# Kernel tuning notes

Measured on AMD Instinct MI355X. Metric: run time of the kernel, lower is better.

The kernel has to match this reference:

```python
import jax, jax.numpy as jnp
import numpy as np

B, T, IN, OUT, H, N, M = 16, 1024, 64, 64, 512, 128, 40
EPS = 1e-8


def setup_inputs() -> dict:
    key = jax.random.key(0)
    ks = jax.random.split(key, 16)
    s = 0.02  # xavier-ish init scale for weights
    inp = {
        "x": jax.random.normal(ks[0], (B, T, IN), jnp.float32),
        "h0": jnp.zeros((B, H), jnp.float32),
        "c0": jnp.zeros((B, H), jnp.float32),
        "memory0": jax.random.normal(ks[1], (B, N, M), jnp.float32) * 0.01,
        "read0": jnp.zeros((B, M), jnp.float32),
        # LSTMCell params (torch gate order: i, f, g, o)
        "W_ih": jax.random.normal(ks[2], (4 * H, IN + M), jnp.float32) * s,
        "b_ih": jnp.zeros((4 * H,), jnp.float32),
        "W_hh": jax.random.normal(ks[3], (4 * H, H), jnp.float32) * s,
        "b_hh": jnp.zeros((4 * H,), jnp.float32),
        "W_fc": jax.random.normal(ks[4], (OUT, H), jnp.float32) * s,
        "b_fc": jnp.zeros((OUT,), jnp.float32),
        "W_e": jax.random.normal(ks[5], (M, H), jnp.float32) * s,
        "b_e": jnp.zeros((M,), jnp.float32),
        "W_a": jax.random.normal(ks[6], (M, H), jnp.float32) * s,
        "b_a": jnp.zeros((M,), jnp.float32),
        "W_k": jax.random.normal(ks[7], (M, H), jnp.float32) * s,
        "b_k": jnp.zeros((M,), jnp.float32),
        "W_b": jax.random.normal(ks[8], (1, H), jnp.float32) * s,
        "b_b": jnp.zeros((1,), jnp.float32),
    }
    return inp


def _ntm_scan(x, h0, c0, memory0, read0, W_ih, b_ih, W_hh, b_hh,
              W_fc, b_fc, W_e, b_e, W_a, b_a, W_k, b_k, W_b, b_b):
    def step(carry, x_t):
        h, c, mem, r = carry
        # controller LSTM cell on [x_t, read_vector]
        inp = jnp.concatenate([x_t, r], axis=-1)            # [B, IN+M]
        gates = inp @ W_ih.T + b_ih + h @ W_hh.T + b_hh      # [B, 4H]
        i, f, g, o = jnp.split(gates, 4, axis=-1)
        i = jax.nn.sigmoid(i); f = jax.nn.sigmoid(f)
        g = jnp.tanh(g);       o = jax.nn.sigmoid(o)
        c = f * c + i * g
        h = o * jnp.tanh(c)
        out = jnp.tanh(h @ W_fc.T + b_fc)                    # [B, OUT]
        # content addressing
        key = jnp.tanh(h @ W_k.T + b_k)                      # [B, M]
        beta = jax.nn.softplus(h @ W_b.T + b_b) + EPS        # [B, 1]
        kn = key / (jnp.linalg.norm(key, axis=-1, keepdims=True) + EPS)
        mn = mem / (jnp.linalg.norm(mem, axis=-1, keepdims=True) + EPS)
        sim = jnp.einsum('bnm,bm->bn', mn, kn)               # [B, N]
        w = jax.nn.softmax(beta * sim, axis=-1)              # [B, N]
        # erase/add write, then read from updated memory
        e = jax.nn.sigmoid(h @ W_e.T + b_e)                  # [B, M]
        a = jnp.tanh(h @ W_a.T + b_a)                        # [B, M]
        mem = mem * (1.0 - w[:, :, None] * e[:, None, :]) + w[:, :, None] * a[:, None, :]
        r = jnp.einsum('bn,bnm->bm', w, mem)                 # [B, M]
        return (h, c, mem, r), out

    xs = jnp.swapaxes(x, 0, 1)                               # [T, B, IN]
    (h, c, mem, r), outs = jax.lax.scan(step, (h0, c0, memory0, read0), xs)
    return jnp.swapaxes(outs, 0, 1), h, c                    # [B, T, OUT]


def reference(x, h0, c0, memory0, read0, W_ih, b_ih, W_hh, b_hh,
              W_fc, b_fc, W_e, b_e, W_a, b_a, W_k, b_k, W_b, b_b):
    return _ntm_scan(x, h0, c0, memory0, read0, W_ih, b_ih, W_hh, b_hh,
                     W_fc, b_fc, W_e, b_e, W_a, b_a, W_k, b_k, W_b, b_b)
```

## Files before the change

### kernel.cpp

```cpp
#include <hip/hip_runtime.h>
#include <math.h>

#define Bq   16
#define Tq   1024
#define INq  64
#define OUTq 64
#define Hq   512
#define Nq   128
#define Mq   40
#define SP   580
#define NWGATE 128
#define NWMEM  16
#define NWG    144
#define NT     512
#define EPSq 1e-8f

typedef unsigned long long ull;

__device__ __forceinline__ float sigmf(float x){ return 1.f/(1.f + expf(-x)); }
__device__ __forceinline__ float softplusf(float x){ return (x > 20.f) ? x : log1pf(expf(x)); }

__device__ __forceinline__ ull icld64(const ull* p){
  return __hip_atomic_load(p, __ATOMIC_RELAXED, __HIP_MEMORY_SCOPE_AGENT);
}
__device__ __forceinline__ void icst64(ull* p, ull v){
  __hip_atomic_store(p, v, __ATOMIC_RELAXED, __HIP_MEMORY_SCOPE_AGENT);
}
__device__ __forceinline__ ull packtv(unsigned tag, float v){
  return ((ull)tag << 32) | (ull)__float_as_uint(v);
}
__device__ __forceinline__ float lowf(ull v){ return __uint_as_float((unsigned)v); }

extern "C" __global__ void __launch_bounds__(NT, 1)
ntm_kernel(const float* __restrict__ xg,  const float* __restrict__ h0g,
           const float* __restrict__ c0g, const float* __restrict__ mem0g,
           const float* __restrict__ read0g,
           const float* __restrict__ Wih, const float* __restrict__ bih,
           const float* __restrict__ Whh, const float* __restrict__ bhh,
           const float* __restrict__ Wfc, const float* __restrict__ bfc,
           const float* __restrict__ We,  const float* __restrict__ be,
           const float* __restrict__ Wa,  const float* __restrict__ ba,
           const float* __restrict__ Wk,  const float* __restrict__ bk,
           const float* __restrict__ Wb,  const float* __restrict__ bbeta,
           float* __restrict__ yout, ull* __restrict__ h_tag,
           ull* __restrict__ r_rep, ull* __restrict__ h_okr)
{
  const int wg  = blockIdx.x;
  const int tid = threadIdx.x;
  __shared__ __align__(16) char smem[60992];

  if (wg < NWGATE){
    float* inp_s  = (float*)smem;
    float* red_s  = (float*)(smem + 37120);
    float* r_s    = (float*)(smem + 54528);
    float* gate_s = (float*)(smem + 57344);
    float* c_s    = (float*)(smem + 58368);
    float* bias_s = (float*)(smem + 58624);
    float* ored_s = (float*)(smem + 58688);

    const int kseg = tid & 15;
    const int rg   = (tid >> 4) & 3;
    const int bg   = tid >> 6;
    const int rep  = wg & 7;

    float4 w4[36];
    #pragma unroll
    for (int g = 0; g < 4; ++g){
      const int row = g*Hq + wg*4 + rg;
      #pragma unroll
      for (int kk = 0; kk < 9; ++kk){
        float v[4];
        #pragma unroll
        for (int c4 = 0; c4 < 4; ++c4){
          const int k = kseg*36 + kk*4 + c4;
          v[c4] = (k < 64) ? Wih[row*104 + k] : Whh[row*512 + (k - 64)];
        }
        w4[g*9 + kk] = make_float4(v[0], v[1], v[2], v[3]);
      }
    }
    float4 wr[10];
    if (tid < 256){
      const int l = tid & 15;
      const int row = (l >> 2)*Hq + wg*4 + (l & 3);
      const float* wir = Wih + row*104 + 64;
      #pragma unroll
      for (int q = 0; q < 10; ++q) wr[q] = *(const float4*)&wir[q*4];
    }
    float4 wf[4]; float bfcv = 0.f;
    if (wg < 64){
      const int ks = tid & 31;
      #pragma unroll
      for (int q = 0; q < 4; ++q)
        wf[q] = *(const float4*)&Wfc[wg*Hq + ks*16 + q*4];
      bfcv = bfc[wg];
    }
    if (tid < 16){
      const int row = (tid >> 2)*Hq + wg*4 + (tid & 3);
      bias_s[tid] = bih[row] + bhh[row];
    }
    if (tid < 64){ const int hh = tid & 3, b = tid >> 2;
      c_s[hh*16 + b] = c0g[b*Hq + wg*4 + hh]; }
    {
      const float4* x4 = (const float4*)xg;
      if (tid < 256){ const int b = tid >> 4, q = tid & 15;
        *(float4*)&inp_s[b*SP + q*4] = x4[(b*Tq + 0)*16 + q]; }
      const float4* h4 = (const float4*)h0g;
      #pragma unroll
      for (int j = 0; j < 4; ++j){ const int i4 = tid + 512*j;
        const int b = i4 >> 7, q = i4 & 127;
        *(float4*)&inp_s[b*SP + 64 + q*4] = h4[b*128 + q]; }
    }
    __syncthreads();

    for (int t = 0; t < Tq; ++t){
      {
        float acc[4][2] = {};
        const float* base = inp_s + kseg*36;
        #pragma unroll
        for (int bl = 0; bl < 2; ++bl){
          const float* bp = base + (2*bg + bl)*SP;
          #pragma unroll
          for (int kk = 0; kk < 9; ++kk){
            const float4 f = *(const float4*)&bp[kk*4];
            #pragma unroll
            for (int g = 0; g < 4; ++g){
              acc[g][bl] += w4[g*9+kk].x*f.x + w4[g*9+kk].y*f.y
                          + w4[g*9+kk].z*f.z + w4[g*9+kk].w*f.w;
            }
          }
        }
        #pragma unroll
        for (int bl = 0; bl < 2; ++bl)
          #pragma unroll
          for (int g = 0; g < 4; ++g)
            red_s[((2*bg + bl)*16 + g*4 + rg)*17 + kseg] = acc[g][bl];
      }
      __syncthreads();
      float part = 0.f;
      if (tid < 256){
        part = bias_s[tid & 15];
        const float* rp = &red_s[tid*17];
        #pragma unroll
        for (int j = 0; j < 16; ++j) part += rp[j];
      }
      if (t == 0){
        if (tid < 320){ const int b = tid/20, mp = tid - b*20;
          *(float2*)&r_s[b*44 + mp*2] = *(const float2*)&read0g[b*40 + mp*2]; }
      } else if (tid < 320){
        const unsigned want = (unsigned)t;
        const ull* rt = r_rep + (ull)(rep*2 + ((t-1)&1))*640;
        ull v1 = icld64(&rt[tid]);
        ull v2 = icld64(&rt[tid + 320]);
        while (((unsigned)(v1 >> 32) != want) | ((unsigned)(v2 >> 32) != want)){
          __builtin_amdgcn_s_sleep(2);
          v1 = icld64(&rt[tid]);
          v2 = icld64(&rt[tid + 320]);
        }
        { const int b = tid/40, m = tid - b*40;       r_s[b*44 + m] = lowf(v1); }
        { const int w = tid + 320, b = w/40, m = w - b*40; r_s[b*44 + m] = lowf(v2); }
      }
      __syncthreads();
      if (tid < 256){
        const int fb = tid >> 4;
        float s = part;
        #pragma unroll
        for (int q = 0; q < 10; ++q){
          const float4 rv = *(const float4*)&r_s[fb*44 + q*4];
          s += wr[q].x*rv.x + wr[q].y*rv.y + wr[q].z*rv.z + wr[q].w*rv.w;
        }
        gate_s[fb*16 + (tid & 15)] = s;
      }
      __syncthreads();
      if (tid < 64){
        const int hh = tid & 3, b = tid >> 2;
        const float gi = gate_s[b*16 + hh];
        const float gf = gate_s[b*16 + 4 + hh];
        const float gc = gate_s[b*16 + 8 + hh];
        const float go = gate_s[b*16 + 12 + hh];
        const float iv = sigmf(gi), fv = sigmf(gf), gv = tanhf(gc), ov = sigmf(go);
        const float cn = fv*c_s[hh*16 + b] + iv*gv;
        const float hn = ov*tanhf(cn);
        c_s[hh*16 + b] = cn;
        icst64(&h_tag[((ull)((t&1)*16 + b))*512 + wg*4 + hh],
               packtv((unsigned)(t+1), hn));
        if (t == Tq - 1){
          yout[Bq*Tq*OUTq + b*Hq + wg*4 + hh] = hn;
          yout[Bq*Tq*OUTq + Bq*Hq + b*Hq + wg*4 + hh] = cn;
        }
      }
      if (wg < 64 && t > 0){
        const int ob = tid >> 5, ks = tid & 31;
        float p = 0.f;
        const float* hp = &inp_s[ob*SP + 64 + ks*16];
        #pragma unroll
        for (int q = 0; q < 4; ++q){
          const float4 f = *(const float4*)&hp[q*4];
          p += wf[q].x*f.x + wf[q].y*f.y + wf[q].z*f.z + wf[q].w*f.w;
        }
        ored_s[ob*36 + ks] = p;
      }
      {
        const unsigned want = (unsigned)(t+1);
        if (tid < 16){
          const ull* fp = &h_okr[(ull)(rep*2 + (t&1))*16 + tid];
          while ((unsigned)(icld64(fp) >> 32) != want)
            __builtin_amdgcn_s_sleep(2);
        }
        __syncthreads();
        const ull* ht = h_tag + (ull)(t&1)*8192;
        ull v[16];
        #pragma unroll
        for (int j = 0; j < 16; ++j) v[j] = icld64(&ht[tid + 512*j]);
        if (wg < 64 && t > 0 && tid < 16){
          const float* op = &ored_s[tid*36];
          float s = bfcv;
          #pragma unroll
          for (int j = 0; j < 32; ++j) s += op[j];
          yout[(tid*Tq + (t-1))*OUTq + wg] = tanhf(s);
        }
        #pragma unroll
        for (int j = 0; j < 16; ++j)
          inp_s[j*SP + 64 + tid] = lowf(v[j]);
      }
      if (t + 1 < Tq && tid < 256){
        const float4* x4 = (const float4*)xg;
        const int b = tid >> 4, q = tid & 15;
        *(float4*)&inp_s[b*SP + q*4] = x4[(b*Tq + (t + 1))*16 + q];
      }
      __syncthreads();
    }
    if (wg < 64){
      const int ob = tid >> 5, ks = tid & 31;
      float p = 0.f;
      const float* hp = &inp_s[ob*SP + 64 + ks*16];
      #pragma unroll
      for (int q = 0; q < 4; ++q){
        const float4 f = *(const float4*)&hp[q*4];
        p += wf[q].x*f.x + wf[q].y*f.y + wf[q].z*f.z + wf[q].w*f.w;
      }
      ored_s[ob*36 + ks] = p;
      __syncthreads();
      if (tid < 16){
        const float* op = &ored_s[tid*36];
        float s = bfcv;
        #pragma unroll
        for (int j = 0; j < 32; ++j) s += op[j];
        yout[(tid*Tq + (Tq-1))*OUTq + wg] = tanhf(s);
      }
    }
  }
  else {
    const int bat = wg - NWGATE;
    float* mem_s  = (float*)smem;
    float* h_s    = (float*)(smem + 22528);
    float* hred_s = (float*)(smem + 24576);
    float* key_s  = (float*)(smem + 26624);
    float* e_s    = (float*)(smem + 26784);
    float* a_s    = (float*)(smem + 26944);
    float* w_s    = (float*)(smem + 27104);
    float* rred_s = (float*)(smem + 27616);

    #pragma unroll
    for (int j = 0; j < 10; ++j){
      const int e = j*512 + tid;
      const int n = e / 40, m = e - n*40;
      mem_s[n*44 + m] = mem0g[bat*(Nq*Mq) + e];
    }
    const int o  = tid & 127;
    const int kc = tid >> 7;
    const float* wrow = (o < 40) ? (Wk + o*Hq)
                      : (o < 80) ? (We + (o-40)*Hq)
                      : (o < 120) ? (Wa + (o-80)*Hq)
                      : (o == 120) ? Wb : nullptr;
    float4 wv2[32];
    if (wrow){
      #pragma unroll
      for (int kk = 0; kk < 32; ++kk)
        wv2[kk] = *(const float4*)&wrow[kc*128 + kk*4];
    } else {
      #pragma unroll
      for (int kk = 0; kk < 32; ++kk) wv2[kk] = make_float4(0.f,0.f,0.f,0.f);
    }
    float hb0 = 0.f, hb1 = 0.f;
    if (tid < 64){
      const int o0 = tid, o1 = tid + 64;
      hb0 = (o0 < 40) ? bk[o0] : be[o0-40];
      hb1 = (o1 < 80) ? be[o1-40] : (o1 < 120) ? ba[o1-80]
          : (o1 == 120) ? bbeta[0] : 0.f;
    }
    __syncthreads();

    for (int t = 0; t < Tq; ++t){
      const int p = t & 1;
      const unsigned want = (unsigned)(t+1);
      {
        const ull* ht = h_tag + ((ull)(p*16 + bat))*512;
        ull v;
        do { v = icld64(&ht[tid]); } while ((unsigned)(v >> 32) != want);
        h_s[tid] = lowf(v);
      }
      __syncthreads();
      if (tid < 8)
        icst64(&h_okr[(ull)(tid*2 + p)*16 + bat], packtv(want, 0.f));
      {
        float a0 = 0.f;
        const float* hp = h_s + kc*128;
        #pragma unroll
        for (int kk = 0; kk < 32; ++kk){
          const float4 f = *(const float4*)&hp[kk*4];
          a0 += wv2[kk].x*f.x + wv2[kk].y*f.y + wv2[kk].z*f.z + wv2[kk].w*f.w;
        }
        hred_s[o*4 + kc] = a0;
      }
      __syncthreads();
      if (tid < 64){
        const int l = tid;
        const float4 p0 = *(const float4*)&hred_s[l*4];
        const float4 p1 = *(const float4*)&hred_s[(l+64)*4];
        float s0 = hb0 + p0.x + p0.y + p0.z + p0.w;
        float s1 = hb1 + p1.x + p1.y + p1.z + p1.w;
        float kv = 0.f;
        if (l < 40){ kv = tanhf(s0); key_s[l] = kv; }
        else        { e_s[l-40] = sigmf(s0); }
        if (l < 16)      e_s[l+24]  = sigmf(s1);
        else if (l < 56) a_s[l-16]  = tanhf(s1);
        float bval = softplusf(s1) + EPSq;
        const float bet = __shfl(bval, 56);
        float ss = kv*kv;
        #pragma unroll
        for (int off = 32; off; off >>= 1) ss += __shfl_xor(ss, off);
        const float rinv = 1.f/(sqrtf(ss) + EPSq);
        float sc[2];
        #pragma unroll
        for (int half = 0; half < 2; ++half){
          const int n = l + 64*half;
          float qq = 0.f, dd = 0.f;
          const float* mrow = &mem_s[n*44];
          #pragma unroll
          for (int q = 0; q < 10; ++q){
            const float4 mv = *(const float4*)&mrow[q*4];
            const float4 kvv = *(const float4*)&key_s[q*4];
            qq += mv.x*mv.x + mv.y*mv.y + mv.z*mv.z + mv.w*mv.w;
            dd += mv.x*kvv.x + mv.y*kvv.y + mv.z*kvv.z + mv.w*kvv.w;
          }
          sc[half] = bet * dd * rinv / (sqrtf(qq) + EPSq);
        }
        float mx = fmaxf(sc[0], sc[1]);
        #pragma unroll
        for (int off = 32; off; off >>= 1) mx = fmaxf(mx, __shfl_xor(mx, off));
        const float e0 = expf(sc[0] - mx), e1 = expf(sc[1] - mx);
        float sm = e0 + e1;
        #pragma unroll
        for (int off = 32; off; off >>= 1) sm += __shfl_xor(sm, off);
        const float inv = 1.f/sm;
        w_s[l] = e0*inv; w_s[l+64] = e1*inv;
      }
      __syncthreads();
      if (tid < 320){
        const int m = tid % 40, ng = tid / 40;
        const float ev = e_s[m], av = a_s[m];
        float part = 0.f;
        #pragma unroll
        for (int j = 0; j < 16; ++j){
          const int n = ng*16 + j, idx = n*44 + m;
          const float mv = mem_s[idx];
          const float wn = w_s[n];
          const float nv = fmaf(wn, fmaf(-ev, mv, av), mv);
          mem_s[idx] = nv;
          part = fmaf(wn, nv, part);
        }
        rred_s[m*9 + ng] = part;
      }
      __syncthreads();
      if (tid < 40){
        float r = 0.f;
        #pragma unroll
        for (int j = 0; j < 8; ++j) r += rred_s[tid*9 + j];
        const ull pv = packtv(want, r);
        #pragma unroll
        for (int rp2 = 0; rp2 < 8; ++rp2)
          icst64(&r_rep[(ull)(rp2*2 + p)*640 + bat*40 + tid], pv);
      }
    }
  }
}

extern "C" void kernel_launch(void* const* d_in, const int* in_sizes, int n_in,
                              void* d_out, int out_size, void* d_ws, size_t ws_size,
                              hipStream_t stream){
  const float* xg    = (const float*)d_in[0];
  const float* h0g   = (const float*)d_in[1];
  const float* c0g   = (const float*)d_in[2];
  const float* mem0g = (const float*)d_in[3];
  const float* read0g= (const float*)d_in[4];
  const float* Wih   = (const float*)d_in[5];
  const float* bih   = (const float*)d_in[6];
  const float* Whh   = (const float*)d_in[7];
  const float* bhh   = (const float*)d_in[8];
  const float* Wfc   = (const float*)d_in[9];
  const float* bfc   = (const float*)d_in[10];
  const float* We    = (const float*)d_in[11];
  const float* be    = (const float*)d_in[12];
  const float* Wa    = (const float*)d_in[13];
  const float* ba    = (const float*)d_in[14];
  const float* Wk    = (const float*)d_in[15];
  const float* bk    = (const float*)d_in[16];
  const float* Wb    = (const float*)d_in[17];
  const float* bbeta = (const float*)d_in[18];

  float* yout  = (float*)d_out;
  ull*   h_tag = (ull*)d_ws;
  ull*   r_rep = (ull*)((char*)d_ws + 131072);
  ull*   h_okr = (ull*)((char*)d_ws + 212992);

  hipMemsetAsync(d_ws, 0, 215040, stream);
  hipLaunchKernelGGL(ntm_kernel, dim3(NWG), dim3(NT), 0, stream,
                     xg, h0g, c0g, mem0g, read0g, Wih, bih, Whh, bhh,
                     Wfc, bfc, We, be, Wa, ba, Wk, bk, Wb, bbeta,
                     yout, h_tag, r_rep, h_okr);
}
```

Measured before the change: 7.000 ms.

## Partition persistent NTM kernel into per-batch islands with local L2 flag exchange

```diff
diff --git a/kernel.cpp b/kernel.cpp
--- a/kernel.cpp
+++ b/kernel.cpp
@@ -3,16 +3,15 @@
 
 #define Bq   16
 #define Tq   1024
-#define INq  64
 #define OUTq 64
 #define Hq   512
 #define Nq   128
 #define Mq   40
-#define SP   580
-#define NWGATE 128
-#define NWMEM  16
-#define NWG    144
-#define NT     512
+#define NT   512
+#define NISL 16
+#define GWG  13
+#define IWG  14
+#define NWG  224
 #define EPSq 1e-8f
 
 typedef unsigned long long ull;
@@ -26,10 +25,34 @@
 __device__ __forceinline__ void icst64(ull* p, ull v){
   __hip_atomic_store(p, v, __ATOMIC_RELAXED, __HIP_MEMORY_SCOPE_AGENT);
 }
+__device__ __forceinline__ ull l2ld64(const ull* p){
+  ull v;
+  asm volatile("global_load_dwordx2 %0, %1, off sc0\n\ts_waitcnt vmcnt(0)"
+               : "=v"(v) : "v"(p) : "memory");
+  return v;
+}
 __device__ __forceinline__ ull packtv(unsigned tag, float v){
   return ((ull)tag << 32) | (ull)__float_as_uint(v);
 }
 __device__ __forceinline__ float lowf(ull v){ return __uint_as_float((unsigned)v); }
+
+__device__ __forceinline__ void publish(ull* loc, ull* sh, ull v){
+  *loc = v;
+  icst64(sh, v);
+}
+__device__ __forceinline__ float waitword(const ull* loc, const ull* sh, unsigned want){
+  #pragma unroll 1
+  for (int i = 0; i < 12; ++i){
+    const ull v = l2ld64(loc);
+    if ((unsigned)(v >> 32) == want) return lowf(v);
+    __builtin_amdgcn_s_sleep(1);
+  }
+  for (;;){
+    const ull v = icld64(sh);
+    if ((unsigned)(v >> 32) == want) return lowf(v);
+    __builtin_amdgcn_s_sleep(2);
+  }
+}
 
 extern "C" __global__ void __launch_bounds__(NT, 1)
 ntm_kernel(const float* __restrict__ xg,  const float* __restrict__ h0g,
@@ -42,215 +65,139 @@
            const float* __restrict__ Wa,  const float* __restrict__ ba,
            const float* __restrict__ Wk,  const float* __restrict__ bk,
            const float* __restrict__ Wb,  const float* __restrict__ bbeta,
-           float* __restrict__ yout, ull* __restrict__ h_tag,
-           ull* __restrict__ r_rep, ull* __restrict__ h_okr)
+           float* __restrict__ yout, ull* __restrict__ rdy,
+           ull* __restrict__ h_loc, ull* __restrict__ h_sh,
+           ull* __restrict__ r_loc, ull* __restrict__ r_sh)
 {
-  const int wg  = blockIdx.x;
+  const int blk = blockIdx.x;
   const int tid = threadIdx.x;
-  __shared__ __align__(16) char smem[60992];
-
-  if (wg < NWGATE){
+  const int x   = blk & 7;
+  const int j   = blk >> 3;
+  const int bat = (j < IWG) ? x : (x + 8);
+  const int slot= (j < IWG) ? j : (j - IWG);
+  __shared__ __align__(16) char smem[41344];
+
+  if (slot < GWG){
     float* inp_s  = (float*)smem;
-    float* red_s  = (float*)(smem + 37120);
-    float* r_s    = (float*)(smem + 54528);
-    float* gate_s = (float*)(smem + 57344);
-    float* c_s    = (float*)(smem + 58368);
-    float* bias_s = (float*)(smem + 58624);
-    float* ored_s = (float*)(smem + 58688);
-
-    const int kseg = tid & 15;
-    const int rg   = (tid >> 4) & 3;
-    const int bg   = tid >> 6;
-    const int rep  = wg & 7;
-
-    float4 w4[36];
+    float* red_s  = (float*)(smem + 2560);
+    float* rw_s   = (float*)(smem + 13440);
+    float* r_s    = (float*)(smem + 39680);
+    float* gate_s = (float*)(smem + 39840);
+    float* c_s    = (float*)(smem + 40480);
+    float* bias_s = (float*)(smem + 40640);
+
+    const int kseg  = tid & 15;
+    const int rslot = tid >> 4;
+    const int nd    = (slot < 12) ? 40 : 32;
+    const int d0    = slot * 40;
+    const int rowsR = 4 * nd;
+
+    float4 w4[5][9];
     #pragma unroll
-    for (int g = 0; g < 4; ++g){
-      const int row = g*Hq + wg*4 + rg;
+    for (int rr = 0; rr < 5; ++rr){
+      const int row = rslot*5 + rr;
+      if (row < rowsR){
+        const int gate = row / nd, ld = row - gate*nd;
+        const int grow = gate*Hq + d0 + ld;
+        #pragma unroll
+        for (int kk = 0; kk < 9; ++kk){
+          float v[4];
+          #pragma unroll
+          for (int c4 = 0; c4 < 4; ++c4){
+            const int k = kseg*36 + kk*4 + c4;
+            v[c4] = (k < 64) ? Wih[grow*104 + k] : Whh[grow*512 + (k - 64)];
+          }
+          w4[rr][kk] = make_float4(v[0], v[1], v[2], v[3]);
+        }
+      } else {
+        #pragma unroll
+        for (int kk = 0; kk < 9; ++kk) w4[rr][kk] = make_float4(0.f,0.f,0.f,0.f);
+      }
+    }
+    if (tid < rowsR){
+      const int gate = tid / nd, ld = tid - gate*nd;
+      const int grow = gate*Hq + d0 + ld;
+      bias_s[tid] = bih[grow] + bhh[grow];
+    }
+    for (int i = tid; i < rowsR*40; i += NT){
+      const int row = i / 40, m = i - row*40;
+      const int gate = row / nd, ld = row - gate*nd;
+      const int grow = gate*Hq + d0 + ld;
+      rw_s[row*41 + m] = Wih[grow*104 + 64 + m];
+    }
+    if (tid < nd) c_s[tid] = c0g[bat*Hq + d0 + tid];
+    if (tid < 16)
+      *(float4*)&inp_s[tid*4] = ((const float4*)xg)[(bat*Tq + 0)*16 + tid];
+    if (tid < 128)
+      *(float4*)&inp_s[64 + tid*4] = ((const float4*)h0g)[bat*128 + tid];
+    __syncthreads();
+    if (tid == 0){
+      __hip_atomic_fetch_add(rdy, 1ull, __ATOMIC_RELAXED, __HIP_MEMORY_SCOPE_AGENT);
+      while (icld64(rdy) < (ull)NWG) __builtin_amdgcn_s_sleep(8);
+    }
+    __syncthreads();
+
+    for (int t = 0; t < Tq; ++t){
+      const int p = t & 1, pm = (t - 1) & 1;
+      float acc[5] = {0.f,0.f,0.f,0.f,0.f};
+      {
+        const float* bp = inp_s + kseg*36;
+        #pragma unroll
+        for (int kk = 0; kk < 9; ++kk){
+          const float4 f = *(const float4*)&bp[kk*4];
+          #pragma unroll
+          for (int rr = 0; rr < 5; ++rr)
+            acc[rr] += w4[rr][kk].x*f.x + w4[rr][kk].y*f.y
+                     + w4[rr][kk].z*f.z + w4[rr][kk].w*f.w;
+        }
+      }
       #pragma unroll
-      for (int kk = 0; kk < 9; ++kk){
-        float v[4];
-        #pragma unroll
-        for (int c4 = 0; c4 < 4; ++c4){
-          const int k = kseg*36 + kk*4 + c4;
-          v[c4] = (k < 64) ? Wih[row*104 + k] : Whh[row*512 + (k - 64)];
-        }
-        w4[g*9 + kk] = make_float4(v[0], v[1], v[2], v[3]);
-      }
-    }
-    float4 wr[10];
-    if (tid < 256){
-      const int l = tid & 15;
-      const int row = (l >> 2)*Hq + wg*4 + (l & 3);
-      const float* wir = Wih + row*104 + 64;
-      #pragma unroll
-      for (int q = 0; q < 10; ++q) wr[q] = *(const float4*)&wir[q*4];
-    }
-    float4 wf[4]; float bfcv = 0.f;
-    if (wg < 64){
-      const int ks = tid & 31;
-      #pragma unroll
-      for (int q = 0; q < 4; ++q)
-        wf[q] = *(const float4*)&Wfc[wg*Hq + ks*16 + q*4];
-      bfcv = bfc[wg];
-    }
-    if (tid < 16){
-      const int row = (tid >> 2)*Hq + wg*4 + (tid & 3);
-      bias_s[tid] = bih[row] + bhh[row];
-    }
-    if (tid < 64){ const int hh = tid & 3, b = tid >> 2;
-      c_s[hh*16 + b] = c0g[b*Hq + wg*4 + hh]; }
-    {
-      const float4* x4 = (const float4*)xg;
-      if (tid < 256){ const int b = tid >> 4, q = tid & 15;
-        *(float4*)&inp_s[b*SP + q*4] = x4[(b*Tq + 0)*16 + q]; }
-      const float4* h4 = (const float4*)h0g;
-      #pragma unroll
-      for (int j = 0; j < 4; ++j){ const int i4 = tid + 512*j;
-        const int b = i4 >> 7, q = i4 & 127;
-        *(float4*)&inp_s[b*SP + 64 + q*4] = h4[b*128 + q]; }
-    }
-    __syncthreads();
-
-    for (int t = 0; t < Tq; ++t){
-      {
-        float acc[4][2] = {};
-        const float* base = inp_s + kseg*36;
-        #pragma unroll
-        for (int bl = 0; bl < 2; ++bl){
-          const float* bp = base + (2*bg + bl)*SP;
-          #pragma unroll
-          for (int kk = 0; kk < 9; ++kk){
-            const float4 f = *(const float4*)&bp[kk*4];
-            #pragma unroll
-            for (int g = 0; g < 4; ++g){
-              acc[g][bl] += w4[g*9+kk].x*f.x + w4[g*9+kk].y*f.y
-                          + w4[g*9+kk].z*f.z + w4[g*9+kk].w*f.w;
-            }
-          }
-        }
-        #pragma unroll
-        for (int bl = 0; bl < 2; ++bl)
-          #pragma unroll
-          for (int g = 0; g < 4; ++g)
-            red_s[((2*bg + bl)*16 + g*4 + rg)*17 + kseg] = acc[g][bl];
-      }
-      __syncthreads();
-      float part = 0.f;
-      if (tid < 256){
-        part = bias_s[tid & 15];
+      for (int rr = 0; rr < 5; ++rr)
+        red_s[(rslot*5 + rr)*17 + kseg] = acc[rr];
+      if (t == 0){
+        if (tid < 40) r_s[tid] = read0g[bat*Mq + tid];
+      } else if (tid < 40){
+        const int idx = (pm*NISL + bat)*Mq + tid;
+        r_s[tid] = waitword(&r_loc[idx], &r_sh[idx], (unsigned)t);
+      }
+      __syncthreads();
+      if (tid < rowsR){
+        float s2 = bias_s[tid];
         const float* rp = &red_s[tid*17];
         #pragma unroll
-        for (int j = 0; j < 16; ++j) part += rp[j];
-      }
-      if (t == 0){
-        if (tid < 320){ const int b = tid/20, mp = tid - b*20;
-          *(float2*)&r_s[b*44 + mp*2] = *(const float2*)&read0g[b*40 + mp*2]; }
-      } else if (tid < 320){
-        const unsigned want = (unsigned)t;
-        const ull* rt = r_rep + (ull)(rep*2 + ((t-1)&1))*640;
-        ull v1 = icld64(&rt[tid]);
-        ull v2 = icld64(&rt[tid + 320]);
-        while (((unsigned)(v1 >> 32) != want) | ((unsigned)(v2 >> 32) != want)){
-          __builtin_amdgcn_s_sleep(2);
-          v1 = icld64(&rt[tid]);
-          v2 = icld64(&rt[tid + 320]);
-        }
-        { const int b = tid/40, m = tid - b*40;       r_s[b*44 + m] = lowf(v1); }
-        { const int w = tid + 320, b = w/40, m = w - b*40; r_s[b*44 + m] = lowf(v2); }
-      }
-      __syncthreads();
-      if (tid < 256){
-        const int fb = tid >> 4;
-        float s = part;
-        #pragma unroll
-        for (int q = 0; q < 10; ++q){
-          const float4 rv = *(const float4*)&r_s[fb*44 + q*4];
-          s += wr[q].x*rv.x + wr[q].y*rv.y + wr[q].z*rv.z + wr[q].w*rv.w;
-        }
-        gate_s[fb*16 + (tid & 15)] = s;
-      }
-      __syncthreads();
-      if (tid < 64){
-        const int hh = tid & 3, b = tid >> 2;
-        const float gi = gate_s[b*16 + hh];
-        const float gf = gate_s[b*16 + 4 + hh];
-        const float gc = gate_s[b*16 + 8 + hh];
-        const float go = gate_s[b*16 + 12 + hh];
+        for (int q = 0; q < 16; ++q) s2 += rp[q];
+        const float* rwp = &rw_s[tid*41];
+        #pragma unroll
+        for (int m = 0; m < 40; ++m) s2 += rwp[m]*r_s[m];
+        gate_s[tid] = s2;
+      }
+      __syncthreads();
+      if (tid < nd){
+        const float gi = gate_s[tid];
+        const float gf = gate_s[nd + tid];
+        const float gc = gate_s[2*nd + tid];
+        const float go = gate_s[3*nd + tid];
         const float iv = sigmf(gi), fv = sigmf(gf), gv = tanhf(gc), ov = sigmf(go);
-        const float cn = fv*c_s[hh*16 + b] + iv*gv;
+        const float cn = fv*c_s[tid] + iv*gv;
         const float hn = ov*tanhf(cn);
-        c_s[hh*16 + b] = cn;
-        icst64(&h_tag[((ull)((t&1)*16 + b))*512 + wg*4 + hh],
-               packtv((unsigned)(t+1), hn));
+        c_s[tid] = cn;
+        const int idx = (p*NISL + bat)*Hq + d0 + tid;
+        publish(&h_loc[idx], &h_sh[idx], packtv((unsigned)(t+1), hn));
         if (t == Tq - 1){
-          yout[Bq*Tq*OUTq + b*Hq + wg*4 + hh] = hn;
-          yout[Bq*Tq*OUTq + Bq*Hq + b*Hq + wg*4 + hh] = cn;
-        }
-      }
-      if (wg < 64 && t > 0){
-        const int ob = tid >> 5, ks = tid & 31;
-        float p = 0.f;
-        const float* hp = &inp_s[ob*SP + 64 + ks*16];
-        #pragma unroll
-        for (int q = 0; q < 4; ++q){
-          const float4 f = *(const float4*)&hp[q*4];
-          p += wf[q].x*f.x + wf[q].y*f.y + wf[q].z*f.z + wf[q].w*f.w;
-        }
-        ored_s[ob*36 + ks] = p;
-      }
-      {
-        const unsigned want = (unsigned)(t+1);
-        if (tid < 16){
-          const ull* fp = &h_okr[(ull)(rep*2 + (t&1))*16 + tid];
-          while ((unsigned)(icld64(fp) >> 32) != want)
-            __builtin_amdgcn_s_sleep(2);
-        }
-        __syncthreads();
-        const ull* ht = h_tag + (ull)(t&1)*8192;
-        ull v[16];
-        #pragma unroll
-        for (int j = 0; j < 16; ++j) v[j] = icld64(&ht[tid + 512*j]);
-        if (wg < 64 && t > 0 && tid < 16){
-          const float* op = &ored_s[tid*36];
-          float s = bfcv;
-          #pragma unroll
-          for (int j = 0; j < 32; ++j) s += op[j];
-          yout[(tid*Tq + (t-1))*OUTq + wg] = tanhf(s);
-        }
-        #pragma unroll
-        for (int j = 0; j < 16; ++j)
-          inp_s[j*SP + 64 + tid] = lowf(v[j]);
-      }
-      if (t + 1 < Tq && tid < 256){
-        const float4* x4 = (const float4*)xg;
-        const int b = tid >> 4, q = tid & 15;
-        *(float4*)&inp_s[b*SP + q*4] = x4[(b*Tq + (t + 1))*16 + q];
-      }
-      __syncthreads();
-    }
-    if (wg < 64){
-      const int ob = tid >> 5, ks = tid & 31;
-      float p = 0.f;
-      const float* hp = &inp_s[ob*SP + 64 + ks*16];
-      #pragma unroll
-      for (int q = 0; q < 4; ++q){
-        const float4 f = *(const float4*)&hp[q*4];
-        p += wf[q].x*f.x + wf[q].y*f.y + wf[q].z*f.z + wf[q].w*f.w;
-      }
-      ored_s[ob*36 + ks] = p;
-      __syncthreads();
-      if (tid < 16){
-        const float* op = &ored_s[tid*36];
-        float s = bfcv;
-        #pragma unroll
-        for (int j = 0; j < 32; ++j) s += op[j];
-        yout[(tid*Tq + (Tq-1))*OUTq + wg] = tanhf(s);
-      }
+          yout[Bq*Tq*OUTq + bat*Hq + d0 + tid] = hn;
+          yout[Bq*Tq*OUTq + Bq*Hq + bat*Hq + d0 + tid] = cn;
+        }
+      }
+      {
+        const int idx = (p*NISL + bat)*Hq + tid;
+        inp_s[64 + tid] = waitword(&h_loc[idx], &h_sh[idx], (unsigned)(t+1));
+      }
+      if (t + 1 < Tq && tid < 16)
+        *(float4*)&inp_s[tid*4] = ((const float4*)xg)[(bat*Tq + t + 1)*16 + tid];
+      __syncthreads();
     }
   }
   else {
-    const int bat = wg - NWGATE;
     float* mem_s  = (float*)smem;
     float* h_s    = (float*)(smem + 22528);
     float* hred_s = (float*)(smem + 24576);
@@ -259,10 +206,11 @@
     float* a_s    = (float*)(smem + 26944);
     float* w_s    = (float*)(smem + 27104);
     float* rred_s = (float*)(smem + 27616);
+    float* ored_s = (float*)(smem + 29056);
 
     #pragma unroll
-    for (int j = 0; j < 10; ++j){
-      const int e = j*512 + tid;
+    for (int q = 0; q < 10; ++q){
+      const int e = q*512 + tid;
       const int n = e / 40, m = e - n*40;
       mem_s[n*44 + m] = mem0g[bat*(Nq*Mq) + e];
     }
@@ -281,6 +229,14 @@
       #pragma unroll
       for (int kk = 0; kk < 32; ++kk) wv2[kk] = make_float4(0.f,0.f,0.f,0.f);
     }
+    float4 wfc[16];
+    {
+      const int o2 = tid & 63, kc8 = tid >> 6;
+      #pragma unroll
+      for (int kk = 0; kk < 16; ++kk)
+        wfc[kk] = *(const float4*)&Wfc[o2*Hq + kc8*64 + kk*4];
+    }
+    const float bfcv = bfc[tid & 63];
     float hb0 = 0.f, hb1 = 0.f;
     if (tid < 64){
       const int o0 = tid, o1 = tid + 64;
@@ -289,19 +245,20 @@
           : (o1 == 120) ? bbeta[0] : 0.f;
     }
     __syncthreads();
+    if (tid == 0){
+      __hip_atomic_fetch_add(rdy, 1ull, __ATOMIC_RELAXED, __HIP_MEMORY_SCOPE_AGENT);
+      while (icld64(rdy) < (ull)NWG) __builtin_amdgcn_s_sleep(8);
+    }
+    __syncthreads();
 
     for (int t = 0; t < Tq; ++t){
       const int p = t & 1;
-      const unsigned want = (unsigned)(t+1);
-      {
-        const ull* ht = h_tag + ((ull)(p*16 + bat))*512;
-        ull v;
-        do { v = icld64(&ht[tid]); } while ((unsigned)(v >> 32) != want);
-        h_s[tid] = lowf(v);
-      }
-      __syncthreads();
-      if (tid < 8)
-        icst64(&h_okr[(ull)(tid*2 + p)*16 + bat], packtv(want, 0.f));
+      const unsigned want = (unsigned)(t + 1);
+      {
+        const int idx = (p*NISL + bat)*Hq + tid;
+        h_s[tid] = waitword(&h_loc[idx], &h_sh[idx], want);
+      }
+      __syncthreads();
       {
         float a0 = 0.f;
         const float* hp = h_s + kc*128;
@@ -361,12 +318,12 @@
         const float ev = e_s[m], av = a_s[m];
         float part = 0.f;
         #pragma unroll
-        for (int j = 0; j < 16; ++j){
-          const int n = ng*16 + j, idx = n*44 + m;
-          const float mv = mem_s[idx];
+        for (int q = 0; q < 16; ++q){
+          const int n = ng*16 + q, idx2 = n*44 + m;
+          const float mv = mem_s[idx2];
           const float wn = w_s[n];
           const float nv = fmaf(wn, fmaf(-ev, mv, av), mv);
-          mem_s[idx] = nv;
+          mem_s[idx2] = nv;
           part = fmaf(wn, nv, part);
         }
         rred_s[m*9 + ng] = part;
@@ -375,12 +332,30 @@
       if (tid < 40){
         float r = 0.f;
         #pragma unroll
-        for (int j = 0; j < 8; ++j) r += rred_s[tid*9 + j];
-        const ull pv = packtv(want, r);
-        #pragma unroll
-        for (int rp2 = 0; rp2 < 8; ++rp2)
-          icst64(&r_rep[(ull)(rp2*2 + p)*640 + bat*40 + tid], pv);
-      }
+        for (int q = 0; q < 8; ++q) r += rred_s[tid*9 + q];
+        const int idx = (p*NISL + bat)*Mq + tid;
+        publish(&r_loc[idx], &r_sh[idx], packtv(want, r));
+      }
+      {
+        const int o2 = tid & 63, kc8 = tid >> 6;
+        float a0 = 0.f;
+        const float* hp = h_s + kc8*64;
+        #pragma unroll
+        for (int kk = 0; kk < 16; ++kk){
+          const float4 f = *(const float4*)&hp[kk*4];
+          a0 += wfc[kk].x*f.x + wfc[kk].y*f.y + wfc[kk].z*f.z + wfc[kk].w*f.w;
+        }
+        ored_s[o2*9 + kc8] = a0;
+      }
+      __syncthreads();
+      if (tid < 64){
+        float s2 = bfcv;
+        const float* op = &ored_s[tid*9];
+        #pragma unroll
+        for (int q = 0; q < 8; ++q) s2 += op[q];
+        yout[(bat*Tq + t)*OUTq + tid] = tanhf(s2);
+      }
+      __syncthreads();
     }
   }
 }
@@ -409,13 +384,15 @@
   const float* bbeta = (const float*)d_in[18];
 
   float* yout  = (float*)d_out;
-  ull*   h_tag = (ull*)d_ws;
-  ull*   r_rep = (ull*)((char*)d_ws + 131072);
-  ull*   h_okr = (ull*)((char*)d_ws + 212992);
-
-  hipMemsetAsync(d_ws, 0, 215040, stream);
+  ull*   rdy   = (ull*)d_ws;
+  ull*   h_loc = (ull*)((char*)d_ws + 4096);
+  ull*   h_sh  = (ull*)((char*)d_ws + 135168);
+  ull*   r_loc = (ull*)((char*)d_ws + 266240);
+  ull*   r_sh  = (ull*)((char*)d_ws + 276480);
+
+  hipMemsetAsync(d_ws, 0, 286720, stream);
   hipLaunchKernelGGL(ntm_kernel, dim3(NWG), dim3(NT), 0, stream,
                      xg, h0g, c0g, mem0g, read0g, Wih, bih, Whh, bhh,
                      Wfc, bfc, We, be, Wa, ba, Wk, bk, Wb, bbeta,
-                     yout, h_tag, r_rep, h_okr);
-}
+                     yout, rdy, h_loc, h_sh, r_loc, r_sh);
+}
```

Result: faster. 6.706 ms (-4.2%).
